# Kernel optimization log

Measured on AMD Instinct MI355X. Metric: run time of the kernel, lower is better.

Reference implementation:

```python
import jax, jax.numpy as jnp
from jax import lax
import numpy as np

N_CLUSTERS = 8
G_CLUSTERS = 2
D_DIM = 512
DN = ('NCHW', 'OIHW', 'NCHW')


def _conv(x, w, b):
    y = lax.conv_general_dilated(x, w, window_strides=(1, 1), padding='VALID',
                                 dimension_numbers=DN)
    return y + b[None, :, None, None]


def setup_inputs() -> dict:
    key = jax.random.key(0)
    ks = jax.random.split(key, 6)
    B, D, H, W = 32, D_DIM, 7, 250
    KG = N_CLUSTERS + G_CLUSTERS
    scale = 1.0 / np.sqrt(D * 7)
    return {
        'x': jax.random.normal(ks[0], (B, D, H, W), dtype=jnp.float32),
        'feat_w': jax.random.normal(ks[1], (D, D, 7, 1), dtype=jnp.float32) * scale,
        'feat_b': jax.random.normal(ks[2], (D,), dtype=jnp.float32) * 0.01,
        'assign_w': jax.random.normal(ks[3], (KG, D, 7, 1), dtype=jnp.float32) * scale,
        'assign_b': jax.random.normal(ks[4], (KG,), dtype=jnp.float32) * 0.01,
        'centroids': jax.random.uniform(ks[5], (D, KG), dtype=jnp.float32),
    }


def reference(x, feat_w, feat_b, assign_w, assign_b, centroids):
    # features branch: conv(7,1) + ReLU -> (B, D, H', W)
    feat = jnp.maximum(_conv(x, feat_w, feat_b), 0.0)
    # assignment branch: conv(7,1) -> softmax over clusters -> (B, K+G, H', W)
    soft = jax.nn.softmax(_conv(x, assign_w, assign_b), axis=1)
    # Fused VLAD aggregation (mathematically identical to
    # sum_hw soft[b,k,hw] * (feat[b,d,hw] - centroids[d,k]) without
    # materializing the (B,D,K+G,H',W) residual tensor):
    s_sum = soft.sum(axis=(-2, -1))                                # (B, K+G)
    agg = jnp.einsum('bkhw,bdhw->bdk', soft, feat)                 # (B, D, K+G)
    cluster_res = agg - centroids[None, :, :] * s_sum[:, None, :]  # (B, D, K+G)
    cluster_res = cluster_res[..., :N_CLUSTERS]                    # drop ghost clusters
    # L2 normalize over feature dim (torch F.normalize, eps=1e-12)
    norm = jnp.sqrt(jnp.sum(cluster_res * cluster_res, axis=1, keepdims=True))
    cluster_l2 = cluster_res / jnp.maximum(norm, 1e-12)
    # (B, D, K) -> (B, K, D) -> (B, K*D)
    out = jnp.swapaxes(cluster_l2, 1, 2).reshape(x.shape[0], N_CLUSTERS * D_DIM)
    return out
```

## Files before the change

### kernel.cpp

```cpp
#include <hip/hip_runtime.h>
#include <stdint.h>

typedef float f32x4 __attribute__((ext_vector_type(4)));
typedef __bf16 bf16x8 __attribute__((ext_vector_type(8)));
typedef unsigned short ushortx8 __attribute__((ext_vector_type(8)));

#define D_DIM 512
#define KGC 10
#define NCLU 8
#define BATCH 32
#define WPOS 250
#define WPAD 256
#define KDIM 3584
#define MROWS 522
#define MPAD 528
#define MBIG 544
#define KSPLIT 4
#define KCHUNK 896
#define NSTEPS 14
#define NTILES 128

__device__ __forceinline__ float bf2f(unsigned short u) {
  union { unsigned int i; float f; } v; v.i = ((unsigned int)u) << 16; return v.f;
}
__device__ __forceinline__ unsigned short f2bf(float f) {
  union { float f; unsigned int i; } v; v.f = f;
  unsigned int r = v.i + 0x7FFFu + ((v.i >> 16) & 1u);
  return (unsigned short)(r >> 16);
}

__device__ __forceinline__ void load_lds16(const void* g, void* l) {
  __builtin_amdgcn_global_load_lds(
      (const __attribute__((address_space(1))) void*)g,
      (__attribute__((address_space(3))) void*)l, 16, 0, 0);
}

__global__ void prep_kernel(const float* __restrict__ fw,
                            const float* __restrict__ fb,
                            const float* __restrict__ aw,
                            const float* __restrict__ ab,
                            unsigned short* __restrict__ Wcat,
                            float* __restrict__ bcat) {
  int r = blockIdx.x;
  unsigned short* dst = Wcat + (size_t)r * KDIM;
  const float* src = (r < D_DIM) ? (fw + (size_t)r * KDIM)
                   : (r < MROWS) ? (aw + (size_t)(r - D_DIM) * KDIM)
                                 : nullptr;
  for (int i = threadIdx.x; i < KDIM / 4; i += 256) {
    unsigned short o0 = 0, o1 = 0, o2 = 0, o3 = 0;
    if (src) {
      float4 v = ((const float4*)src)[i];
      o0 = f2bf(v.x); o1 = f2bf(v.y); o2 = f2bf(v.z); o3 = f2bf(v.w);
    }
    ushort4 o; o.x = o0; o.y = o1; o.z = o2; o.w = o3;
    ((ushort4*)dst)[i] = o;
  }
  if (threadIdx.x == 0)
    bcat[r] = r < D_DIM ? fb[r] : (r < MROWS ? ab[r - D_DIM] : 0.f);
}

__global__ __launch_bounds__(256, 2) void gemm_fused(
    const float* __restrict__ x, const unsigned short* __restrict__ Wcat,
    float* __restrict__ P) {
  __shared__ __align__(16) unsigned short Wl[MBIG * 64];
  __shared__ __align__(16) unsigned short Xl[64 * 64];
  const int tid = threadIdx.x;
  const int nt = blockIdx.x, sp = blockIdx.y;
  const int b = nt >> 2, n0 = (nt & 3) * 64;
  const int lane = tid & 63, wv = tid >> 6;
  const int fr = lane & 15, kg = lane >> 4;
  const int sx = fr & 7;
  const int nloc = tid & 63;
  const int nglob = n0 + nloc;
  const bool okn = nglob < WPOS;
  const int kb0 = tid >> 6;
  const float* xb = x + (size_t)b * KDIM * WPOS + nglob;
  const int kbase = sp * KCHUNK;

  float vx[16];
#pragma unroll
  for (int pass = 0; pass < 2; pass++) {
    int kb = kb0 + 4 * pass;
#pragma unroll
    for (int e = 0; e < 8; e++) {
      int k = kbase + kb * 8 + e;
      vx[pass * 8 + e] = okn ? xb[(size_t)k * WPOS] : 0.f;
    }
  }

  const f32x4 zero = {0.f, 0.f, 0.f, 0.f};
  f32x4 acc[8][4];
#pragma unroll
  for (int i = 0; i < 8; i++)
#pragma unroll
    for (int j = 0; j < 4; j++) acc[i][j] = zero;
  f32x4 acca = zero;

  for (int st = 0; st < NSTEPS; st++) {
    const int kst = kbase + st * 64;
    __syncthreads();
#pragma unroll
    for (int pass = 0; pass < 2; pass++) {
      int kb = kb0 + 4 * pass;
      ushortx8 pk;
#pragma unroll
      for (int e = 0; e < 8; e++) pk[e] = f2bf(vx[pass * 8 + e]);
      *(ushortx8*)&Xl[nloc * 64 + (kb ^ (nloc & 7)) * 8] = pk;
    }
#pragma unroll
    for (int it = 0; it < 17; it++) {
      int s = it * 256 + tid;
      int row = s >> 3, p = s & 7;
      int blk = p ^ (row & 7);
      load_lds16(Wcat + (size_t)row * KDIM + kst + blk * 8, &Wl[s * 8]);
    }
    __syncthreads();
    if (st + 1 < NSTEPS) {
      const int kst2 = kst + 64;
#pragma unroll
      for (int pass = 0; pass < 2; pass++) {
        int kb = kb0 + 4 * pass;
#pragma unroll
        for (int e = 0; e < 8; e++) {
          int k = kst2 + kb * 8 + e;
          vx[pass * 8 + e] = okn ? xb[(size_t)k * WPOS] : 0.f;
        }
      }
    }
#pragma unroll
    for (int ks = 0; ks < 64; ks += 32) {
      const int off = (((ks >> 3) + kg) ^ sx) * 8;
      bf16x8 bfr[4];
#pragma unroll
      for (int j = 0; j < 4; j++)
        bfr[j] = *(const bf16x8*)&Xl[(j * 16 + fr) * 64 + off];
      {
        bf16x8 aas = *(const bf16x8*)&Wl[(512 + fr) * 64 + off];
        bf16x8 bfa = *(const bf16x8*)&Xl[(wv * 16 + fr) * 64 + off];
        acca = __builtin_amdgcn_mfma_f32_16x16x32_bf16(aas, bfa, acca, 0, 0, 0);
      }
#pragma unroll
      for (int i = 0; i < 8; i++) {
        bf16x8 af = *(const bf16x8*)&Wl[(wv * 128 + i * 16 + fr) * 64 + off];
#pragma unroll
        for (int j = 0; j < 4; j++)
          acc[i][j] = __builtin_amdgcn_mfma_f32_16x16x32_bf16(af, bfr[j], acc[i][j], 0, 0, 0);
      }
    }
  }

  float* Pb = P + (size_t)(sp * NTILES + nt) * (MBIG * 64);
#pragma unroll
  for (int i = 0; i < 8; i++) {
#pragma unroll
    for (int r = 0; r < 4; r++) {
      int m = wv * 128 + i * 16 + kg * 4 + r;
#pragma unroll
      for (int j = 0; j < 4; j++)
        Pb[(size_t)m * 64 + j * 16 + fr] = acc[i][j][r];
    }
  }
#pragma unroll
  for (int r = 0; r < 4; r++)
    Pb[(size_t)(512 + kg * 4 + r) * 64 + wv * 16 + fr] = acca[r];
}

__global__ __launch_bounds__(256) void reduce_kernel(
    const float* __restrict__ P, const float* __restrict__ bcat,
    unsigned short* __restrict__ Y) {
  const int nt = blockIdx.x, mg = blockIdx.y;
  const int t = threadIdx.x;
  const int m = mg * 32 + (t >> 3);
  const int nl = (t & 7) * 8;
  if (m >= MPAD) return;
  const size_t base = (size_t)nt * (MBIG * 64) + (size_t)m * 64 + nl;
  const size_t spstr = (size_t)NTILES * (MBIG * 64);
  float s[8];
#pragma unroll
  for (int e = 0; e < 8; e++) s[e] = 0.f;
#pragma unroll
  for (int sp = 0; sp < KSPLIT; sp++) {
    const float* p = P + sp * spstr + base;
    float4 a = *(const float4*)p;
    float4 c = *(const float4*)(p + 4);
    s[0] += a.x; s[1] += a.y; s[2] += a.z; s[3] += a.w;
    s[4] += c.x; s[5] += c.y; s[6] += c.z; s[7] += c.w;
  }
  float bias = bcat[m];
  ushortx8 o;
#pragma unroll
  for (int e = 0; e < 8; e++) {
    float v = s[e] + bias;
    if (m < D_DIM) v = fmaxf(v, 0.f);
    o[e] = f2bf(v);
  }
  const int bb = nt >> 2, c0 = (nt & 3) * 64 + nl;
  *(ushortx8*)&Y[(size_t)bb * MPAD * WPAD + (size_t)m * WPAD + c0] = o;
}

__global__ __launch_bounds__(256) void epi_kernel(
    const unsigned short* __restrict__ Y, const float* __restrict__ cent,
    float* __restrict__ out) {
  __shared__ float soft[WPAD];
  __shared__ float red[4];
  const int b = blockIdx.x >> 3, k = blockIdx.x & 7;
  const int tid = threadIdx.x;
  const unsigned short* Yb = Y + (size_t)b * MPAD * WPAD;

  float sv = 0.f;
  if (tid < WPOS) {
    float lg[KGC];
    float mx = -1e30f;
#pragma unroll
    for (int j = 0; j < KGC; j++) {
      lg[j] = bf2f(Yb[(size_t)(D_DIM + j) * WPAD + tid]);
      mx = fmaxf(mx, lg[j]);
    }
    float s = 0.f, ek = 0.f;
#pragma unroll
    for (int j = 0; j < KGC; j++) {
      float e = __expf(lg[j] - mx);
      s += e;
      if (j == k) ek = e;
    }
    sv = ek / s;
  }
  soft[tid] = sv;
  __syncthreads();

  float v = sv;
#pragma unroll
  for (int o = 32; o > 0; o >>= 1) v += __shfl_down(v, o, 64);
  if ((tid & 63) == 0) red[tid >> 6] = v;
  __syncthreads();
  float ssum = red[0] + red[1] + red[2] + red[3];

  float a0 = 0.f, a1 = 0.f;
  const unsigned short* row0 = Yb + (size_t)tid * WPAD;
  const unsigned short* row1 = Yb + (size_t)(tid + 256) * WPAD;
  for (int w = 0; w < WPAD; w += 8) {
    ushortx8 f0 = *(const ushortx8*)(row0 + w);
    ushortx8 f1 = *(const ushortx8*)(row1 + w);
#pragma unroll
    for (int u = 0; u < 8; u++) {
      float s = soft[w + u];
      a0 += bf2f(f0[u]) * s;
      a1 += bf2f(f1[u]) * s;
    }
  }
  float c0 = a0 - cent[(size_t)tid * KGC + k] * ssum;
  float c1 = a1 - cent[(size_t)(tid + 256) * KGC + k] * ssum;

  __syncthreads();
  float q = c0 * c0 + c1 * c1;
#pragma unroll
  for (int o = 32; o > 0; o >>= 1) q += __shfl_down(q, o, 64);
  if ((tid & 63) == 0) red[tid >> 6] = q;
  __syncthreads();
  float norm = sqrtf(red[0] + red[1] + red[2] + red[3]);
  float inv = 1.f / fmaxf(norm, 1e-12f);

  float* ob = out + (size_t)b * (NCLU * D_DIM) + (size_t)k * D_DIM;
  ob[tid] = c0 * inv;
  ob[tid + 256] = c1 * inv;
}

extern "C" void kernel_launch(void* const* d_in, const int* in_sizes, int n_in,
                              void* d_out, int out_size, void* d_ws, size_t ws_size,
                              hipStream_t stream) {
  const float* x  = (const float*)d_in[0];
  const float* fw = (const float*)d_in[1];
  const float* fb = (const float*)d_in[2];
  const float* aw = (const float*)d_in[3];
  const float* ab = (const float*)d_in[4];
  const float* ce = (const float*)d_in[5];
  float* out = (float*)d_out;
  char* ws = (char*)d_ws;

  const size_t WC_BYTES = (size_t)640 * KDIM * 2;
  const size_t BC_BYTES = 4096;
  const size_t P_BYTES  = (size_t)KSPLIT * NTILES * MBIG * 64 * 4;
  unsigned short* Wc = (unsigned short*)(ws);
  float*          bc = (float*)(ws + WC_BYTES);
  float*          P  = (float*)(ws + WC_BYTES + BC_BYTES);
  unsigned short* Yv = (unsigned short*)(ws + WC_BYTES + BC_BYTES + P_BYTES);

  prep_kernel<<<MBIG, 256, 0, stream>>>(fw, fb, aw, ab, Wc, bc);
  gemm_fused<<<dim3(NTILES, KSPLIT), 256, 0, stream>>>(x, Wc, P);
  reduce_kernel<<<dim3(NTILES, 17), 256, 0, stream>>>(P, bc, Yv);
  epi_kernel<<<BATCH * NCLU, 256, 0, stream>>>(Yv, ce, out);
}
```

Before: 255.6 us.

## Double-buffer GEMM LDS tiles with 512-thread blocks and halve the K-split

The fused GEMM moves to 512-thread blocks with double-buffered LDS for both the weight and the activation tiles. The weight DMA for step st+2 and the x global loads for step st+3 are issued while the current step computes, so there is one barrier per step instead of two. The K-split drops from 4 to 2, which halves the partial-sum traffic through P, and each wave now owns a 272x16 output slice. In exchange, A fragments are reused less, so LDS read traffic rises. The roughly 155KB of LDS also limits each CU to one block, cutting occupancy and leaving only 256 blocks in the grid.

```diff
diff --git a/kernel.cpp b/kernel.cpp
--- a/kernel.cpp
+++ b/kernel.cpp
@@ -15,9 +15,9 @@
 #define MROWS 522
 #define MPAD 528
 #define MBIG 544
-#define KSPLIT 4
-#define KCHUNK 896
-#define NSTEPS 14
+#define KSPLIT 2
+#define KCHUNK 1792
+#define NS 28
 #define NTILES 128
 
 __device__ __forceinline__ float bf2f(unsigned short u) {
@@ -59,110 +59,91 @@
     bcat[r] = r < D_DIM ? fb[r] : (r < MROWS ? ab[r - D_DIM] : 0.f);
 }
 
-__global__ __launch_bounds__(256, 2) void gemm_fused(
+__global__ __launch_bounds__(512, 2) void gemm_fused(
     const float* __restrict__ x, const unsigned short* __restrict__ Wcat,
     float* __restrict__ P) {
-  __shared__ __align__(16) unsigned short Wl[MBIG * 64];
-  __shared__ __align__(16) unsigned short Xl[64 * 64];
+  __shared__ __align__(16) unsigned short Wl[2][MBIG * 64];
+  __shared__ __align__(16) unsigned short Xl[2][64 * 64];
   const int tid = threadIdx.x;
   const int nt = blockIdx.x, sp = blockIdx.y;
   const int b = nt >> 2, n0 = (nt & 3) * 64;
   const int lane = tid & 63, wv = tid >> 6;
   const int fr = lane & 15, kg = lane >> 4;
   const int sx = fr & 7;
-  const int nloc = tid & 63;
+  const int mh = (wv & 1) * 272;
+  const int nq = wv >> 1;
+  const int nloc = tid & 63, kb = tid >> 6;
   const int nglob = n0 + nloc;
   const bool okn = nglob < WPOS;
-  const int kb0 = tid >> 6;
   const float* xb = x + (size_t)b * KDIM * WPOS + nglob;
   const int kbase = sp * KCHUNK;
 
-  float vx[16];
-#pragma unroll
-  for (int pass = 0; pass < 2; pass++) {
-    int kb = kb0 + 4 * pass;
-#pragma unroll
-    for (int e = 0; e < 8; e++) {
-      int k = kbase + kb * 8 + e;
-      vx[pass * 8 + e] = okn ? xb[(size_t)k * WPOS] : 0.f;
-    }
-  }
-
+  float xr[2][8];
+  auto loadx = [&](int st, float* dst) {
+    int k0 = kbase + st * 64 + kb * 8;
+#pragma unroll
+    for (int e = 0; e < 8; e++)
+      dst[e] = okn ? xb[(size_t)(k0 + e) * WPOS] : 0.f;
+  };
+  auto dma_w = [&](int buf, int st) {
+    int kst = kbase + st * 64;
+#pragma unroll
+    for (int it = 0; it < 9; it++) {
+      int s = it * 512 + tid;
+      if (s < MBIG * 8) {
+        int row = s >> 3, p = s & 7;
+        int blk = p ^ (row & 7);
+        load_lds16(Wcat + (size_t)row * KDIM + kst + blk * 8, &Wl[buf][s * 8]);
+      }
+    }
+  };
+  auto write_x = [&](int buf, const float* src) {
+    ushortx8 pk;
+#pragma unroll
+    for (int e = 0; e < 8; e++) pk[e] = f2bf(src[e]);
+    *(ushortx8*)&Xl[buf][nloc * 64 + (kb ^ (nloc & 7)) * 8] = pk;
+  };
+
+  f32x4 acc[17];
   const f32x4 zero = {0.f, 0.f, 0.f, 0.f};
-  f32x4 acc[8][4];
-#pragma unroll
-  for (int i = 0; i < 8; i++)
-#pragma unroll
-    for (int j = 0; j < 4; j++) acc[i][j] = zero;
-  f32x4 acca = zero;
-
-  for (int st = 0; st < NSTEPS; st++) {
-    const int kst = kbase + st * 64;
+#pragma unroll
+  for (int f = 0; f < 17; f++) acc[f] = zero;
+
+  loadx(0, xr[0]);
+  loadx(1, xr[1]);
+  dma_w(0, 0);
+  write_x(0, xr[0]);
+  loadx(2, xr[0]);
+  __syncthreads();
+  dma_w(1, 1);
+
+  for (int st = 0; st < NS; st++) {
+    const int cur = st & 1, nxt = cur ^ 1;
+    if (st + 1 < NS) write_x(nxt, xr[nxt]);
+    if (st + 3 < NS) loadx(st + 3, xr[nxt]);
+#pragma unroll
+    for (int ks = 0; ks < 2; ks++) {
+      const int off = ((ks * 4 + kg) ^ sx) * 8;
+      bf16x8 bfr = *(const bf16x8*)&Xl[cur][(nq * 16 + fr) * 64 + off];
+#pragma unroll
+      for (int f = 0; f < 17; f++) {
+        bf16x8 af = *(const bf16x8*)&Wl[cur][(mh + f * 16 + fr) * 64 + off];
+        acc[f] = __builtin_amdgcn_mfma_f32_16x16x32_bf16(af, bfr, acc[f], 0, 0, 0);
+      }
+    }
     __syncthreads();
-#pragma unroll
-    for (int pass = 0; pass < 2; pass++) {
-      int kb = kb0 + 4 * pass;
-      ushortx8 pk;
-#pragma unroll
-      for (int e = 0; e < 8; e++) pk[e] = f2bf(vx[pass * 8 + e]);
-      *(ushortx8*)&Xl[nloc * 64 + (kb ^ (nloc & 7)) * 8] = pk;
-    }
-#pragma unroll
-    for (int it = 0; it < 17; it++) {
-      int s = it * 256 + tid;
-      int row = s >> 3, p = s & 7;
-      int blk = p ^ (row & 7);
-      load_lds16(Wcat + (size_t)row * KDIM + kst + blk * 8, &Wl[s * 8]);
-    }
-    __syncthreads();
-    if (st + 1 < NSTEPS) {
-      const int kst2 = kst + 64;
-#pragma unroll
-      for (int pass = 0; pass < 2; pass++) {
-        int kb = kb0 + 4 * pass;
-#pragma unroll
-        for (int e = 0; e < 8; e++) {
-          int k = kst2 + kb * 8 + e;
-          vx[pass * 8 + e] = okn ? xb[(size_t)k * WPOS] : 0.f;
-        }
-      }
-    }
-#pragma unroll
-    for (int ks = 0; ks < 64; ks += 32) {
-      const int off = (((ks >> 3) + kg) ^ sx) * 8;
-      bf16x8 bfr[4];
-#pragma unroll
-      for (int j = 0; j < 4; j++)
-        bfr[j] = *(const bf16x8*)&Xl[(j * 16 + fr) * 64 + off];
-      {
-        bf16x8 aas = *(const bf16x8*)&Wl[(512 + fr) * 64 + off];
-        bf16x8 bfa = *(const bf16x8*)&Xl[(wv * 16 + fr) * 64 + off];
-        acca = __builtin_amdgcn_mfma_f32_16x16x32_bf16(aas, bfa, acca, 0, 0, 0);
-      }
-#pragma unroll
-      for (int i = 0; i < 8; i++) {
-        bf16x8 af = *(const bf16x8*)&Wl[(wv * 128 + i * 16 + fr) * 64 + off];
-#pragma unroll
-        for (int j = 0; j < 4; j++)
-          acc[i][j] = __builtin_amdgcn_mfma_f32_16x16x32_bf16(af, bfr[j], acc[i][j], 0, 0, 0);
-      }
-    }
+    if (st + 2 < NS) dma_w(cur, st + 2);
   }
 
   float* Pb = P + (size_t)(sp * NTILES + nt) * (MBIG * 64);
-#pragma unroll
-  for (int i = 0; i < 8; i++) {
-#pragma unroll
-    for (int r = 0; r < 4; r++) {
-      int m = wv * 128 + i * 16 + kg * 4 + r;
-#pragma unroll
-      for (int j = 0; j < 4; j++)
-        Pb[(size_t)m * 64 + j * 16 + fr] = acc[i][j][r];
-    }
-  }
-#pragma unroll
-  for (int r = 0; r < 4; r++)
-    Pb[(size_t)(512 + kg * 4 + r) * 64 + wv * 16 + fr] = acca[r];
+  const int n = nq * 16 + fr;
+#pragma unroll
+  for (int f = 0; f < 17; f++) {
+    const int m = mh + f * 16 + kg * 4;
+#pragma unroll
+    for (int r = 0; r < 4; r++)
+      Pb[(size_t)(m + r) * 64 + n] = acc[f][r];
+  }
 }
 
 __global__ __launch_bounds__(256) void reduce_kernel(
@@ -277,7 +258,7 @@
   float* out = (float*)d_out;
   char* ws = (char*)d_ws;
 
-  const size_t WC_BYTES = (size_t)640 * KDIM * 2;
+  const size_t WC_BYTES = (size_t)MBIG * KDIM * 2;
   const size_t BC_BYTES = 4096;
   const size_t P_BYTES  = (size_t)KSPLIT * NTILES * MBIG * 64 * 4;
   unsigned short* Wc = (unsigned short*)(ws);
@@ -286,7 +267,7 @@
   unsigned short* Yv = (unsigned short*)(ws + WC_BYTES + BC_BYTES + P_BYTES);
 
   prep_kernel<<<MBIG, 256, 0, stream>>>(fw, fb, aw, ab, Wc, bc);
-  gemm_fused<<<dim3(NTILES, KSPLIT), 256, 0, stream>>>(x, Wc, P);
+  gemm_fused<<<dim3(NTILES, KSPLIT), 512, 0, stream>>>(x, Wc, P);
   reduce_kernel<<<dim3(NTILES, 17), 256, 0, stream>>>(P, bc, Yv);
   epi_kernel<<<BATCH * NCLU, 256, 0, stream>>>(Yv, ce, out);
 }
```

Result: slower. 309.9 us (+21.2%).
